# Kernel tuning notes

Hardware: AMD Instinct MI355X
Metric: run time of the kernel (lower is better)

## Reference

```python
import jax, jax.numpy as jnp
import numpy as np

NUM_NODES = 100000
EMB_DIM = 64
NUM_LAYERS = 3
DROPOUT_P = 0.1
NUM_EDGES = 1200000


def setup_inputs() -> dict:
    key = jax.random.key(0)
    k1, k2 = jax.random.split(key)
    # Xavier-uniform init for the embedding table (as in the torch module)
    limit = (6.0 / (NUM_NODES + EMB_DIM)) ** 0.5
    emb_weight = jax.random.uniform(k1, (NUM_NODES, EMB_DIM), jnp.float32, -limit, limit)
    edge_index = jax.random.randint(k2, (2, NUM_EDGES), 0, NUM_NODES, dtype=jnp.int32)
    return {"emb_weight": emb_weight, "edge_index": edge_index}


def _lightgcn(x, edge_index):
    # Standard LightGCN propagation: x_{l+1} = A_hat x_l with symmetric norm,
    # output = mean over layer embeddings 0..L.
    src, dst = edge_index[0], edge_index[1]
    ones = jnp.ones((edge_index.shape[1],), dtype=x.dtype)
    deg = jax.ops.segment_sum(ones, dst, num_segments=NUM_NODES)
    deg_inv_sqrt = jnp.where(deg > 0, jax.lax.rsqrt(jnp.maximum(deg, 1.0)), 0.0)
    norm = deg_inv_sqrt[src] * deg_inv_sqrt[dst]  # [E]
    out = x
    acc = x
    for _ in range(NUM_LAYERS):
        msg = out[src] * norm[:, None]                       # gather [E, D]
        out = jax.ops.segment_sum(msg, dst, num_segments=NUM_NODES)  # scatter-add [N, D]
        acc = acc + out
    return acc / (NUM_LAYERS + 1)


def _dropout(x, p, key):
    keep = jax.random.bernoulli(key, 1.0 - p, x.shape)
    return jnp.where(keep, x / (1.0 - p), jnp.zeros((), x.dtype))


def reference(emb_weight, edge_index):
    out = _lightgcn(emb_weight, edge_index)
    # Dropout in train mode, fixed key for reproducibility
    return _dropout(out, DROPOUT_P, jax.random.key(42))
```

## Files before the change

kernel.cpp:

```cpp
#include <hip/hip_runtime.h>
#include <hip/hip_fp16.h>
#include <math.h>

#define N_NODES 100000
#define EMB 64
#define N_EDGES 1200000
#define N_ELEM (N_NODES * EMB)
#define SCAN_CHUNK 1024
#define SCAN_NBLK ((N_NODES + SCAN_CHUNK - 1) / SCAN_CHUNK)
#define NPART 8
#define PART_SIZE (N_NODES / NPART)
#define SC_GRID 1024
#define SC_TPB 256

__device__ __forceinline__ unsigned rotl32(unsigned v, int r) {
    return (v << r) | (v >> (32 - r));
}

__device__ __forceinline__ void threefry2x32(unsigned k0, unsigned k1,
                                             unsigned c0, unsigned c1,
                                             unsigned& o0, unsigned& o1) {
    const unsigned ks0 = k0;
    const unsigned ks1 = k1;
    const unsigned ks2 = k0 ^ k1 ^ 0x1BD11BDAu;
    unsigned x0 = c0 + ks0;
    unsigned x1 = c1 + ks1;
#define TF_RND(r) { x0 += x1; x1 = rotl32(x1, r); x1 ^= x0; }
    TF_RND(13) TF_RND(15) TF_RND(26) TF_RND(6)
    x0 += ks1; x1 += ks2 + 1u;
    TF_RND(17) TF_RND(29) TF_RND(16) TF_RND(24)
    x0 += ks2; x1 += ks0 + 2u;
    TF_RND(13) TF_RND(15) TF_RND(26) TF_RND(6)
    x0 += ks0; x1 += ks1 + 3u;
    TF_RND(17) TF_RND(29) TF_RND(16) TF_RND(24)
    x0 += ks1; x1 += ks2 + 4u;
    TF_RND(13) TF_RND(15) TF_RND(26) TF_RND(6)
    x0 += ks2; x1 += ks0 + 5u;
#undef TF_RND
    o0 = x0;
    o1 = x1;
}

__device__ __forceinline__ bool drop_keep(unsigned i) {
    unsigned o0, o1;
    threefry2x32(0u, 42u, 0u, i, o0, o1);
    unsigned bits = o0 ^ o1;
    float u = __uint_as_float((bits >> 9) | 0x3f800000u) - 1.0f;
    return u < 0.9f;
}

__global__ void k_cvt(const float* __restrict__ in, __half* __restrict__ out) {
    int base = (blockIdx.x * blockDim.x + threadIdx.x) * 8;
    if (base >= N_ELEM) return;
    const float4 f0 = *reinterpret_cast<const float4*>(in + base);
    const float4 f1 = *reinterpret_cast<const float4*>(in + base + 4);
    __half2 h0 = __float22half2_rn(make_float2(f0.x, f0.y));
    __half2 h1 = __float22half2_rn(make_float2(f0.z, f0.w));
    __half2 h2 = __float22half2_rn(make_float2(f1.x, f1.y));
    __half2 h3 = __float22half2_rn(make_float2(f1.z, f1.w));
    uint4 u;
    u.x = *(unsigned*)&h0; u.y = *(unsigned*)&h1;
    u.z = *(unsigned*)&h2; u.w = *(unsigned*)&h3;
    *reinterpret_cast<uint4*>(out + base) = u;
}

__global__ void k_hist(const int* __restrict__ dst, int* __restrict__ cnt) {
    int e = blockIdx.x * blockDim.x + threadIdx.x;
    if (e < N_EDGES) atomicAdd(&cnt[dst[e]], 1);
}

__global__ void k_scan1(const int* __restrict__ cnt, int* __restrict__ local,
                        int* __restrict__ bsum, float* __restrict__ dis) {
    __shared__ int wsum[16];
    const int tid = threadIdx.x;
    const int lane = tid & 63;
    const int wid = tid >> 6;
    int i = blockIdx.x * SCAN_CHUNK + tid;
    int v = (i < N_NODES) ? cnt[i] : 0;
    if (i < N_NODES) dis[i] = (v > 0) ? rsqrtf((float)v) : 0.0f;
    int x = v;
#pragma unroll
    for (int off = 1; off < 64; off <<= 1) {
        int t = __shfl_up(x, off, 64);
        if (lane >= off) x += t;
    }
    if (lane == 63) wsum[wid] = x;
    __syncthreads();
    if (wid == 0 && lane < 16) {
        int w = wsum[lane];
#pragma unroll
        for (int off = 1; off < 16; off <<= 1) {
            int t = __shfl_up(w, off, 64);
            if (lane >= off) w += t;
        }
        wsum[lane] = w;
    }
    __syncthreads();
    int wexc = (wid == 0) ? 0 : wsum[wid - 1];
    if (i < N_NODES) local[i] = (x + wexc) - v;
    if (tid == 0) bsum[blockIdx.x] = wsum[15];
}

__global__ void k_scan2(const int* __restrict__ bsum, int* __restrict__ bofs) {
    __shared__ int sh[128];
    int t = threadIdx.x;
    int v = (t < SCAN_NBLK) ? bsum[t] : 0;
    sh[t] = v;
    __syncthreads();
    for (int off = 1; off < 128; off <<= 1) {
        int add = (t >= off) ? sh[t - off] : 0;
        __syncthreads();
        sh[t] += add;
        __syncthreads();
    }
    if (t < SCAN_NBLK) bofs[t] = sh[t] - v;
}

__global__ void k_scan3(int* __restrict__ cursor_local, const int* __restrict__ bofs,
                        int* __restrict__ rowptr) {
    int i = blockIdx.x * SCAN_CHUNK + threadIdx.x;
    if (i < N_NODES) {
        int r = cursor_local[i] + bofs[blockIdx.x];
        rowptr[i] = r;
        cursor_local[i] = r;
    }
    if (i == 0) rowptr[N_NODES] = N_EDGES;
}

__global__ void k_scatter(const int* __restrict__ src, const int* __restrict__ dst,
                          const float* __restrict__ dis, int* __restrict__ cursor,
                          int2* __restrict__ edges) {
    const int p = blockIdx.x & (NPART - 1);
    const int lo = p * PART_SIZE;
    const int hi = lo + PART_SIZE;
    const int stride = (SC_GRID / NPART) * SC_TPB;
    int e = (blockIdx.x >> 3) * SC_TPB + threadIdx.x;
    for (; e < N_EDGES; e += stride) {
        int d = dst[e];
        if (d >= lo && d < hi) {
            int s = src[e];
            int pos = atomicAdd(&cursor[d], 1);
            edges[pos] = make_int2(s, __float_as_int(dis[s] * dis[d]));
        }
    }
}

__device__ __forceinline__ float4 h4_to_f4(uint2 u) {
    __half2 p = *(__half2*)&u.x, q = *(__half2*)&u.y;
    float2 a = __half22float2(p), b = __half22float2(q);
    return make_float4(a.x, a.y, b.x, b.y);
}

template <int MODE>
__global__ void k_agg(const int* __restrict__ rowptr, const int2* __restrict__ edges,
                      const __half* __restrict__ x, __half* __restrict__ y,
                      const float* __restrict__ own, float* __restrict__ acc) {
    const int gwid = (blockIdx.x * blockDim.x + threadIdx.x) >> 6;
    const int lane = threadIdx.x & 63;
    const int g = lane >> 4;
    const int l16 = lane & 15;
    const int n = (gwid << 2) + g;
    if (n >= N_NODES) return;
    const int begin = rowptr[n];
    const int end = rowptr[n + 1];
    const __half* xb = x + (l16 << 2);
    float4 s = make_float4(0.f, 0.f, 0.f, 0.f);
    int j = begin;
    for (; j + 3 < end; j += 4) {
        int2 r0 = edges[j];
        int2 r1 = edges[j + 1];
        int2 r2 = edges[j + 2];
        int2 r3 = edges[j + 3];
        uint2 u0 = *reinterpret_cast<const uint2*>(xb + (size_t)r0.x * EMB);
        uint2 u1 = *reinterpret_cast<const uint2*>(xb + (size_t)r1.x * EMB);
        uint2 u2 = *reinterpret_cast<const uint2*>(xb + (size_t)r2.x * EMB);
        uint2 u3 = *reinterpret_cast<const uint2*>(xb + (size_t)r3.x * EMB);
        float4 v0 = h4_to_f4(u0), v1 = h4_to_f4(u1), v2 = h4_to_f4(u2), v3 = h4_to_f4(u3);
        float n0 = __int_as_float(r0.y), n1 = __int_as_float(r1.y);
        float n2 = __int_as_float(r2.y), n3 = __int_as_float(r3.y);
        s.x += v0.x * n0 + v1.x * n1 + v2.x * n2 + v3.x * n3;
        s.y += v0.y * n0 + v1.y * n1 + v2.y * n2 + v3.y * n3;
        s.z += v0.z * n0 + v1.z * n1 + v2.z * n2 + v3.z * n3;
        s.w += v0.w * n0 + v1.w * n1 + v2.w * n2 + v3.w * n3;
    }
    for (; j < end; ++j) {
        int2 r0 = edges[j];
        float n0 = __int_as_float(r0.y);
        float4 v0 = h4_to_f4(*reinterpret_cast<const uint2*>(xb + (size_t)r0.x * EMB));
        s.x += v0.x * n0; s.y += v0.y * n0; s.z += v0.z * n0; s.w += v0.w * n0;
    }
    const size_t ridx = (size_t)n * EMB + (l16 << 2);
    if (MODE == 0 || MODE == 1) {
        __half2 h0 = __float22half2_rn(make_float2(s.x, s.y));
        __half2 h1 = __float22half2_rn(make_float2(s.z, s.w));
        uint2 u;
        u.x = *(unsigned*)&h0; u.y = *(unsigned*)&h1;
        *reinterpret_cast<uint2*>(y + ridx) = u;
        if (MODE == 0) {
            float4 o = *reinterpret_cast<const float4*>(own + ridx);
            *reinterpret_cast<float4*>(acc + ridx) =
                make_float4(o.x + s.x, o.y + s.y, o.z + s.z, o.w + s.w);
        } else {
            float4 a = *reinterpret_cast<const float4*>(acc + ridx);
            *reinterpret_cast<float4*>(acc + ridx) =
                make_float4(a.x + s.x, a.y + s.y, a.z + s.z, a.w + s.w);
        }
    } else {
        float4 a = *reinterpret_cast<const float4*>(acc + ridx);
        float4 t = make_float4(a.x + s.x, a.y + s.y, a.z + s.z, a.w + s.w);
        const float sc = 0.25f / 0.9f;
        unsigned base = (unsigned)ridx;
        float4 o;
        o.x = drop_keep(base + 0u) ? t.x * sc : 0.f;
        o.y = drop_keep(base + 1u) ? t.y * sc : 0.f;
        o.z = drop_keep(base + 2u) ? t.z * sc : 0.f;
        o.w = drop_keep(base + 3u) ? t.w * sc : 0.f;
        *reinterpret_cast<float4*>(acc + ridx) = o;
    }
}

extern "C" void kernel_launch(void* const* d_in, const int* in_sizes, int n_in,
                              void* d_out, int out_size, void* d_ws, size_t ws_size,
                              hipStream_t stream) {
    const float* emb = (const float*)d_in[0];
    const int* eidx = (const int*)d_in[1];
    const int* src = eidx;
    const int* dst = eidx + N_EDGES;
    float* acc = (float*)d_out;

    char* ws = (char*)d_ws;
    int*    cnt     = (int*)(ws + 0);
    int*    cursor  = (int*)(ws + 400000);
    int*    bsum    = (int*)(ws + 800000);
    int*    bofs    = (int*)(ws + 800400);
    int*    rowptr  = (int*)(ws + 800800);
    float*  dis     = (float*)(ws + 1200808);
    int2*   edges   = (int2*)(ws + 1600808);
    __half* embh    = (__half*)(ws + 11200816);
    __half* bufAh   = (__half*)(ws + 24000832);
    __half* bufBh   = (__half*)(ws + 36800832);

    const int BLK = 256;
    const int gE   = (N_EDGES + BLK - 1) / BLK;
    const int gCvt = (N_ELEM / 8 + BLK - 1) / BLK;
    const int gAgg = ((N_NODES + 3) / 4 * 64 + BLK - 1) / BLK;

    k_cvt<<<gCvt, BLK, 0, stream>>>(emb, embh);

    hipMemsetAsync(cnt, 0, N_NODES * sizeof(int), stream);
    k_hist<<<gE, BLK, 0, stream>>>(dst, cnt);
    k_scan1<<<SCAN_NBLK, SCAN_CHUNK, 0, stream>>>(cnt, cursor, bsum, dis);
    k_scan2<<<1, 128, 0, stream>>>(bsum, bofs);
    k_scan3<<<SCAN_NBLK, SCAN_CHUNK, 0, stream>>>(cursor, bofs, rowptr);
    k_scatter<<<SC_GRID, SC_TPB, 0, stream>>>(src, dst, dis, cursor, edges);

    k_agg<0><<<gAgg, BLK, 0, stream>>>(rowptr, edges, embh,  bufAh, emb, acc);
    k_agg<1><<<gAgg, BLK, 0, stream>>>(rowptr, edges, bufAh, bufBh, nullptr, acc);
    k_agg<2><<<gAgg, BLK, 0, stream>>>(rowptr, edges, bufBh, nullptr, nullptr, acc);
}
```

Baseline: 324.8 us.

## Factor symmetric normalization into node scaling and store source-only CSR edges

Rewrites propagation as z = D^-1/2 x, so each edge needs only its source index and the per-edge weight multiply goes away. The edge array shrinks from int2 to int, the scatter kernel reads dst and src four at a time and doubles its grid, and the aggregation loop is unrolled to eight. This targets edge-stream bandwidth and multiply work in the three gather passes, at the cost of an extra dis[n] scaling per node and fp16 storage of pre-scaled values, which changes rounding slightly.

```diff
diff --git a/kernel.cpp b/kernel.cpp
--- a/kernel.cpp
+++ b/kernel.cpp
@@ -10,7 +10,7 @@
 #define SCAN_NBLK ((N_NODES + SCAN_CHUNK - 1) / SCAN_CHUNK)
 #define NPART 8
 #define PART_SIZE (N_NODES / NPART)
-#define SC_GRID 1024
+#define SC_GRID 2048
 #define SC_TPB 256
 
 __device__ __forceinline__ unsigned rotl32(unsigned v, int r) {
@@ -49,21 +49,6 @@
     return u < 0.9f;
 }
 
-__global__ void k_cvt(const float* __restrict__ in, __half* __restrict__ out) {
-    int base = (blockIdx.x * blockDim.x + threadIdx.x) * 8;
-    if (base >= N_ELEM) return;
-    const float4 f0 = *reinterpret_cast<const float4*>(in + base);
-    const float4 f1 = *reinterpret_cast<const float4*>(in + base + 4);
-    __half2 h0 = __float22half2_rn(make_float2(f0.x, f0.y));
-    __half2 h1 = __float22half2_rn(make_float2(f0.z, f0.w));
-    __half2 h2 = __float22half2_rn(make_float2(f1.x, f1.y));
-    __half2 h3 = __float22half2_rn(make_float2(f1.z, f1.w));
-    uint4 u;
-    u.x = *(unsigned*)&h0; u.y = *(unsigned*)&h1;
-    u.z = *(unsigned*)&h2; u.w = *(unsigned*)&h3;
-    *reinterpret_cast<uint4*>(out + base) = u;
-}
-
 __global__ void k_hist(const int* __restrict__ dst, int* __restrict__ cnt) {
     int e = blockIdx.x * blockDim.x + threadIdx.x;
     if (e < N_EDGES) atomicAdd(&cnt[dst[e]], 1);
@@ -127,21 +112,37 @@
     if (i == 0) rowptr[N_NODES] = N_EDGES;
 }
 
+__global__ void k_cvt(const float* __restrict__ emb, const float* __restrict__ dis,
+                      __half* __restrict__ z0) {
+    int base = (blockIdx.x * blockDim.x + threadIdx.x) * 8;
+    if (base >= N_ELEM) return;
+    float d = dis[base >> 6];
+    const float4 f0 = *reinterpret_cast<const float4*>(emb + base);
+    const float4 f1 = *reinterpret_cast<const float4*>(emb + base + 4);
+    __half2 h0 = __float22half2_rn(make_float2(f0.x * d, f0.y * d));
+    __half2 h1 = __float22half2_rn(make_float2(f0.z * d, f0.w * d));
+    __half2 h2 = __float22half2_rn(make_float2(f1.x * d, f1.y * d));
+    __half2 h3 = __float22half2_rn(make_float2(f1.z * d, f1.w * d));
+    uint4 u;
+    u.x = *(unsigned*)&h0; u.y = *(unsigned*)&h1;
+    u.z = *(unsigned*)&h2; u.w = *(unsigned*)&h3;
+    *reinterpret_cast<uint4*>(z0 + base) = u;
+}
+
 __global__ void k_scatter(const int* __restrict__ src, const int* __restrict__ dst,
-                          const float* __restrict__ dis, int* __restrict__ cursor,
-                          int2* __restrict__ edges) {
+                          int* __restrict__ cursor, int* __restrict__ edges) {
     const int p = blockIdx.x & (NPART - 1);
     const int lo = p * PART_SIZE;
     const int hi = lo + PART_SIZE;
-    const int stride = (SC_GRID / NPART) * SC_TPB;
-    int e = (blockIdx.x >> 3) * SC_TPB + threadIdx.x;
+    const int stride = (SC_GRID / NPART) * SC_TPB * 4;
+    int e = (((blockIdx.x >> 3) * SC_TPB) + threadIdx.x) * 4;
     for (; e < N_EDGES; e += stride) {
-        int d = dst[e];
-        if (d >= lo && d < hi) {
-            int s = src[e];
-            int pos = atomicAdd(&cursor[d], 1);
-            edges[pos] = make_int2(s, __float_as_int(dis[s] * dis[d]));
-        }
+        const int4 d4 = *reinterpret_cast<const int4*>(dst + e);
+        const int4 s4 = *reinterpret_cast<const int4*>(src + e);
+        if (d4.x >= lo && d4.x < hi) edges[atomicAdd(&cursor[d4.x], 1)] = s4.x;
+        if (d4.y >= lo && d4.y < hi) edges[atomicAdd(&cursor[d4.y], 1)] = s4.y;
+        if (d4.z >= lo && d4.z < hi) edges[atomicAdd(&cursor[d4.z], 1)] = s4.z;
+        if (d4.w >= lo && d4.w < hi) edges[atomicAdd(&cursor[d4.w], 1)] = s4.w;
     }
 }
 
@@ -152,8 +153,9 @@
 }
 
 template <int MODE>
-__global__ void k_agg(const int* __restrict__ rowptr, const int2* __restrict__ edges,
-                      const __half* __restrict__ x, __half* __restrict__ y,
+__global__ void k_agg(const int* __restrict__ rowptr, const int* __restrict__ edges,
+                      const float* __restrict__ dis,
+                      const __half* __restrict__ z, __half* __restrict__ znext,
                       const float* __restrict__ own, float* __restrict__ acc) {
     const int gwid = (blockIdx.x * blockDim.x + threadIdx.x) >> 6;
     const int lane = threadIdx.x & 63;
@@ -163,51 +165,62 @@
     if (n >= N_NODES) return;
     const int begin = rowptr[n];
     const int end = rowptr[n + 1];
-    const __half* xb = x + (l16 << 2);
+    const __half* zb = z + (l16 << 2);
     float4 s = make_float4(0.f, 0.f, 0.f, 0.f);
     int j = begin;
+    for (; j + 7 < end; j += 8) {
+        int e0 = edges[j],     e1 = edges[j + 1], e2 = edges[j + 2], e3 = edges[j + 3];
+        int e4 = edges[j + 4], e5 = edges[j + 5], e6 = edges[j + 6], e7 = edges[j + 7];
+        float4 v0 = h4_to_f4(*reinterpret_cast<const uint2*>(zb + (size_t)e0 * EMB));
+        float4 v1 = h4_to_f4(*reinterpret_cast<const uint2*>(zb + (size_t)e1 * EMB));
+        float4 v2 = h4_to_f4(*reinterpret_cast<const uint2*>(zb + (size_t)e2 * EMB));
+        float4 v3 = h4_to_f4(*reinterpret_cast<const uint2*>(zb + (size_t)e3 * EMB));
+        float4 v4 = h4_to_f4(*reinterpret_cast<const uint2*>(zb + (size_t)e4 * EMB));
+        float4 v5 = h4_to_f4(*reinterpret_cast<const uint2*>(zb + (size_t)e5 * EMB));
+        float4 v6 = h4_to_f4(*reinterpret_cast<const uint2*>(zb + (size_t)e6 * EMB));
+        float4 v7 = h4_to_f4(*reinterpret_cast<const uint2*>(zb + (size_t)e7 * EMB));
+        s.x += ((v0.x + v1.x) + (v2.x + v3.x)) + ((v4.x + v5.x) + (v6.x + v7.x));
+        s.y += ((v0.y + v1.y) + (v2.y + v3.y)) + ((v4.y + v5.y) + (v6.y + v7.y));
+        s.z += ((v0.z + v1.z) + (v2.z + v3.z)) + ((v4.z + v5.z) + (v6.z + v7.z));
+        s.w += ((v0.w + v1.w) + (v2.w + v3.w)) + ((v4.w + v5.w) + (v6.w + v7.w));
+    }
     for (; j + 3 < end; j += 4) {
-        int2 r0 = edges[j];
-        int2 r1 = edges[j + 1];
-        int2 r2 = edges[j + 2];
-        int2 r3 = edges[j + 3];
-        uint2 u0 = *reinterpret_cast<const uint2*>(xb + (size_t)r0.x * EMB);
-        uint2 u1 = *reinterpret_cast<const uint2*>(xb + (size_t)r1.x * EMB);
-        uint2 u2 = *reinterpret_cast<const uint2*>(xb + (size_t)r2.x * EMB);
-        uint2 u3 = *reinterpret_cast<const uint2*>(xb + (size_t)r3.x * EMB);
-        float4 v0 = h4_to_f4(u0), v1 = h4_to_f4(u1), v2 = h4_to_f4(u2), v3 = h4_to_f4(u3);
-        float n0 = __int_as_float(r0.y), n1 = __int_as_float(r1.y);
-        float n2 = __int_as_float(r2.y), n3 = __int_as_float(r3.y);
-        s.x += v0.x * n0 + v1.x * n1 + v2.x * n2 + v3.x * n3;
-        s.y += v0.y * n0 + v1.y * n1 + v2.y * n2 + v3.y * n3;
-        s.z += v0.z * n0 + v1.z * n1 + v2.z * n2 + v3.z * n3;
-        s.w += v0.w * n0 + v1.w * n1 + v2.w * n2 + v3.w * n3;
+        int e0 = edges[j], e1 = edges[j + 1], e2 = edges[j + 2], e3 = edges[j + 3];
+        float4 v0 = h4_to_f4(*reinterpret_cast<const uint2*>(zb + (size_t)e0 * EMB));
+        float4 v1 = h4_to_f4(*reinterpret_cast<const uint2*>(zb + (size_t)e1 * EMB));
+        float4 v2 = h4_to_f4(*reinterpret_cast<const uint2*>(zb + (size_t)e2 * EMB));
+        float4 v3 = h4_to_f4(*reinterpret_cast<const uint2*>(zb + (size_t)e3 * EMB));
+        s.x += (v0.x + v1.x) + (v2.x + v3.x);
+        s.y += (v0.y + v1.y) + (v2.y + v3.y);
+        s.z += (v0.z + v1.z) + (v2.z + v3.z);
+        s.w += (v0.w + v1.w) + (v2.w + v3.w);
     }
     for (; j < end; ++j) {
-        int2 r0 = edges[j];
-        float n0 = __int_as_float(r0.y);
-        float4 v0 = h4_to_f4(*reinterpret_cast<const uint2*>(xb + (size_t)r0.x * EMB));
-        s.x += v0.x * n0; s.y += v0.y * n0; s.z += v0.z * n0; s.w += v0.w * n0;
-    }
+        float4 v0 = h4_to_f4(*reinterpret_cast<const uint2*>(zb + (size_t)edges[j] * EMB));
+        s.x += v0.x; s.y += v0.y; s.z += v0.z; s.w += v0.w;
+    }
+    const float dn = dis[n];
+    const float4 out = make_float4(s.x * dn, s.y * dn, s.z * dn, s.w * dn);
     const size_t ridx = (size_t)n * EMB + (l16 << 2);
     if (MODE == 0 || MODE == 1) {
-        __half2 h0 = __float22half2_rn(make_float2(s.x, s.y));
-        __half2 h1 = __float22half2_rn(make_float2(s.z, s.w));
+        const float dn2 = dn * dn;
+        __half2 h0 = __float22half2_rn(make_float2(s.x * dn2, s.y * dn2));
+        __half2 h1 = __float22half2_rn(make_float2(s.z * dn2, s.w * dn2));
         uint2 u;
         u.x = *(unsigned*)&h0; u.y = *(unsigned*)&h1;
-        *reinterpret_cast<uint2*>(y + ridx) = u;
+        *reinterpret_cast<uint2*>(znext + ridx) = u;
         if (MODE == 0) {
             float4 o = *reinterpret_cast<const float4*>(own + ridx);
             *reinterpret_cast<float4*>(acc + ridx) =
-                make_float4(o.x + s.x, o.y + s.y, o.z + s.z, o.w + s.w);
+                make_float4(o.x + out.x, o.y + out.y, o.z + out.z, o.w + out.w);
         } else {
             float4 a = *reinterpret_cast<const float4*>(acc + ridx);
             *reinterpret_cast<float4*>(acc + ridx) =
-                make_float4(a.x + s.x, a.y + s.y, a.z + s.z, a.w + s.w);
+                make_float4(a.x + out.x, a.y + out.y, a.z + out.z, a.w + out.w);
         }
     } else {
         float4 a = *reinterpret_cast<const float4*>(acc + ridx);
-        float4 t = make_float4(a.x + s.x, a.y + s.y, a.z + s.z, a.w + s.w);
+        float4 t = make_float4(a.x + out.x, a.y + out.y, a.z + out.z, a.w + out.w);
         const float sc = 0.25f / 0.9f;
         unsigned base = (unsigned)ridx;
         float4 o;
@@ -235,26 +248,25 @@
     int*    bofs    = (int*)(ws + 800400);
     int*    rowptr  = (int*)(ws + 800800);
     float*  dis     = (float*)(ws + 1200808);
-    int2*   edges   = (int2*)(ws + 1600808);
-    __half* embh    = (__half*)(ws + 11200816);
-    __half* bufAh   = (__half*)(ws + 24000832);
-    __half* bufBh   = (__half*)(ws + 36800832);
+    int*    edges   = (int*)(ws + 1600808);
+    __half* z0      = (__half*)(ws + 6400816);
+    __half* z1      = (__half*)(ws + 19200816);
+    __half* z2      = (__half*)(ws + 32000816);
 
     const int BLK = 256;
     const int gE   = (N_EDGES + BLK - 1) / BLK;
     const int gCvt = (N_ELEM / 8 + BLK - 1) / BLK;
     const int gAgg = ((N_NODES + 3) / 4 * 64 + BLK - 1) / BLK;
-
-    k_cvt<<<gCvt, BLK, 0, stream>>>(emb, embh);
 
     hipMemsetAsync(cnt, 0, N_NODES * sizeof(int), stream);
     k_hist<<<gE, BLK, 0, stream>>>(dst, cnt);
     k_scan1<<<SCAN_NBLK, SCAN_CHUNK, 0, stream>>>(cnt, cursor, bsum, dis);
     k_scan2<<<1, 128, 0, stream>>>(bsum, bofs);
     k_scan3<<<SCAN_NBLK, SCAN_CHUNK, 0, stream>>>(cursor, bofs, rowptr);
-    k_scatter<<<SC_GRID, SC_TPB, 0, stream>>>(src, dst, dis, cursor, edges);
-
-    k_agg<0><<<gAgg, BLK, 0, stream>>>(rowptr, edges, embh,  bufAh, emb, acc);
-    k_agg<1><<<gAgg, BLK, 0, stream>>>(rowptr, edges, bufAh, bufBh, nullptr, acc);
-    k_agg<2><<<gAgg, BLK, 0, stream>>>(rowptr, edges, bufBh, nullptr, nullptr, acc);
-}
+    k_cvt<<<gCvt, BLK, 0, stream>>>(emb, dis, z0);
+    k_scatter<<<SC_GRID, SC_TPB, 0, stream>>>(src, dst, cursor, edges);
+
+    k_agg<0><<<gAgg, BLK, 0, stream>>>(rowptr, edges, dis, z0, z1, emb, acc);
+    k_agg<1><<<gAgg, BLK, 0, stream>>>(rowptr, edges, dis, z1, z2, nullptr, acc);
+    k_agg<2><<<gAgg, BLK, 0, stream>>>(rowptr, edges, dis, z2, nullptr, nullptr, acc);
+}
```

Result: no change. 326.4 us (+0.5%).
